# Kernel optimization log

Measured on AMD Instinct MI355X. Metric: run time of the kernel, lower is better.

## Reference

```python
import jax, jax.numpy as jnp
import numpy as np

H = 64
VOCAB = 64
THRESH_SCALE = 0.4
LN_EPS = 1e-5
NORM_EPS = 1e-12


def setup_inputs() -> dict:
    key = jax.random.key(0)
    ks = jax.random.split(key, 16)
    B, L = 64, 1024
    s = 1.0 / np.sqrt(H)
    inp = {
        "seq": jax.random.randint(ks[0], (B, L), 0, VOCAB),
        "embed_W": jax.random.normal(ks[1], (VOCAB, H), jnp.float32),
        "ff_W1": jax.random.normal(ks[2], (H, 2 * H), jnp.float32) * s,
        "ff_b1": jnp.zeros((2 * H,), jnp.float32),
        "ff_W2": jax.random.normal(ks[3], (2 * H, H), jnp.float32) * s,
        "ff_b2": jnp.zeros((H,), jnp.float32),
        "ln_g": jnp.ones((H,), jnp.float32),
        "ln_b": jnp.zeros((H,), jnp.float32),
        "kp_W": jax.random.normal(ks[4], (H, H), jnp.float32) * s,
        "vp_W": jax.random.normal(ks[5], (H, H), jnp.float32) * s,
        "qp_W": jax.random.normal(ks[6], (H, H), jnp.float32) * s,
        "rp_W": jax.random.normal(ks[7], (H, H), jnp.float32) * s,
        "rp_b": jnp.zeros((H,), jnp.float32),
        "out_W": jax.random.normal(ks[8], (H, VOCAB), jnp.float32) * s,
        "out_b": jnp.zeros((VOCAB,), jnp.float32),
    }
    return inp


def _forward(seq, embed_W, ff_W1, ff_b1, ff_W2, ff_b2, ln_g, ln_b,
             kp_W, vp_W, qp_W, rp_W, rp_b, out_W, out_b):
    h = embed_W[seq]                                    # [B, L, H]
    ff = jnp.maximum(h @ ff_W1 + ff_b1, 0.0) @ ff_W2 + ff_b2
    x = h + ff
    mu = x.mean(-1, keepdims=True)
    var = ((x - mu) ** 2).mean(-1, keepdims=True)       # biased var (torch LayerNorm)
    hn = (x - mu) / jnp.sqrt(var + LN_EPS) * ln_g + ln_b
    B, L, _ = hn.shape

    # Precompute all per-step keys/values, then scan the fast-weight update.
    k_all = hn[:, :-1] @ kp_W                           # [B, L-1, H]
    v_all = hn[:, :-1] @ vp_W                           # [B, L-1, H]
    kn_all = k_all / jnp.maximum(
        jnp.linalg.norm(k_all, axis=-1, keepdims=True), NORM_EPS)

    def step(M, kv):
        kn, v = kv                                      # each [B, H]
        vp = jnp.einsum('bij,bj->bi', M, kn)            # read M along k
        err = jnp.linalg.norm(v - vp, axis=-1)          # [B]
        gate = jnp.where(err > THRESH_SCALE * jnp.linalg.norm(v, axis=-1),
                         1.0, 0.0)                      # hard energy gate
        M = M + gate[:, None, None] * jnp.einsum('bi,bj->bij', v - vp, kn)
        return M, None

    M0 = jnp.zeros((B, H, H), dtype=hn.dtype)
    M, _ = jax.lax.scan(step, M0,
                        (kn_all.transpose(1, 0, 2), v_all.transpose(1, 0, 2)))

    q = hn[:, -1] @ qp_W                                # [B, H]
    r = jnp.einsum('bij,bj->bi', M, q) @ rp_W + rp_b
    return r @ out_W + out_b                            # [B, VOCAB]


def reference(seq, embed_W, ff_W1, ff_b1, ff_W2, ff_b2, ln_g, ln_b,
              kp_W, vp_W, qp_W, rp_W, rp_b, out_W, out_b):
    return _forward(seq, embed_W, ff_W1, ff_b1, ff_W2, ff_b2, ln_g, ln_b,
                    kp_W, vp_W, qp_W, rp_W, rp_b, out_W, out_b)
```

## Files before the change

### kernel.cpp

```cpp
#include <hip/hip_runtime.h>
#include <hip/hip_bf16.h>
#include <math.h>

#define BB 64
#define LL 1024
#define HH 64

typedef float v4f __attribute__((ext_vector_type(4)));
#define F4 __builtin_elementwise_fma

__global__ __launch_bounds__(256, 1)
void token_kernel(const int* __restrict__ seq,
                  const float* __restrict__ embed_W,
                  const float* __restrict__ ff_W1, const float* __restrict__ ff_b1,
                  const float* __restrict__ ff_W2, const float* __restrict__ ff_b2,
                  const float* __restrict__ ln_g, const float* __restrict__ ln_b,
                  const float* __restrict__ kp_W, const float* __restrict__ vp_W,
                  const float* __restrict__ qp_W,
                  float* __restrict__ knv, float* __restrict__ vthr,
                  float* __restrict__ qbuf)
{
    __shared__ __align__(16) float h_s[32][64];
    __shared__ __align__(16) float t1_s[32][128];
    __shared__ __align__(16) float hn_s[32][64];

    const int tid  = threadIdx.x;
    const int tok0 = blockIdx.x * 32;

#pragma unroll
    for (int k = 0; k < 8; ++k) {
        int e   = k * 256 + tid;
        int tok = e >> 6, i = e & 63;
        int s   = seq[tok0 + tok];
        h_s[tok][i] = embed_W[s * 64 + i];
    }
    __syncthreads();

    {
        const int j = tid & 127;
        const int g = tid >> 7;
        float w1c[64];
#pragma unroll
        for (int ii = 0; ii < 64; ++ii) w1c[ii] = ff_W1[ii * 128 + j];
        const float b1j = ff_b1[j];
#pragma unroll
        for (int tk = 0; tk < 16; ++tk) {
            const int tok = g * 16 + tk;
            const float4* h4 = (const float4*)h_s[tok];
            float a0 = b1j, a1 = 0.f, a2 = 0.f, a3 = 0.f;
#pragma unroll
            for (int w = 0; w < 16; ++w) {
                float4 hv = h4[w];
                a0 = fmaf(hv.x, w1c[4*w+0], a0);
                a1 = fmaf(hv.y, w1c[4*w+1], a1);
                a2 = fmaf(hv.z, w1c[4*w+2], a2);
                a3 = fmaf(hv.w, w1c[4*w+3], a3);
            }
            t1_s[tok][j] = fmaxf((a0 + a1) + (a2 + a3), 0.f);
        }
    }
    __syncthreads();

    {
        const int i  = tid & 63;
        const int w4 = tid >> 6;
        const float b2i = ff_b2[i];
        const float gi  = ln_g[i];
        const float bi  = ln_b[i];
        float accf[8];
#pragma unroll
        for (int tk = 0; tk < 8; ++tk) accf[tk] = b2i;
#pragma unroll
        for (int h = 0; h < 2; ++h) {
            float w2c[64];
#pragma unroll
            for (int jj = 0; jj < 64; ++jj) w2c[jj] = ff_W2[(h*64 + jj) * 64 + i];
#pragma unroll
            for (int tk = 0; tk < 8; ++tk) {
                const int tok = w4 * 8 + tk;
                const float4* t4 = (const float4*)&t1_s[tok][h*64];
                float a0 = 0.f, a1 = 0.f, a2 = 0.f, a3 = 0.f;
#pragma unroll
                for (int w = 0; w < 16; ++w) {
                    float4 tv = t4[w];
                    a0 = fmaf(tv.x, w2c[4*w+0], a0);
                    a1 = fmaf(tv.y, w2c[4*w+1], a1);
                    a2 = fmaf(tv.z, w2c[4*w+2], a2);
                    a3 = fmaf(tv.w, w2c[4*w+3], a3);
                }
                accf[tk] += (a0 + a1) + (a2 + a3);
            }
        }
#pragma unroll
        for (int tk = 0; tk < 8; ++tk) {
            const int tok = w4 * 8 + tk;
            float x = h_s[tok][i] + accf[tk];
            float s = x;
#pragma unroll
            for (int m = 32; m > 0; m >>= 1) s += __shfl_xor(s, m);
            float mu = s * (1.f / 64.f);
            float d  = x - mu;
            float s2 = d * d;
#pragma unroll
            for (int m = 32; m > 0; m >>= 1) s2 += __shfl_xor(s2, m);
            float var = s2 * (1.f / 64.f);
            hn_s[tok][i] = d / sqrtf(var + 1e-5f) * gi + bi;
        }
    }
    __syncthreads();

    {
        const int i  = tid & 63;
        const int w4 = tid >> 6;
        float kc[64], vc[64];
#pragma unroll
        for (int ii = 0; ii < 64; ++ii) {
            kc[ii] = kp_W[ii * 64 + i];
            vc[ii] = vp_W[ii * 64 + i];
        }
#pragma unroll
        for (int tk = 0; tk < 8; ++tk) {
            const int tok = w4 * 8 + tk;
            const int tg  = tok0 + tok;
            const int b   = tg >> 10;
            const int t   = tg & 1023;
            const float4* hn4 = (const float4*)hn_s[tok];
            if (t < 1023) {
                float ka0=0.f,ka1=0.f,ka2=0.f,ka3=0.f;
                float va0=0.f,va1=0.f,va2=0.f,va3=0.f;
#pragma unroll
                for (int w = 0; w < 16; ++w) {
                    float4 hv = hn4[w];
                    ka0 = fmaf(hv.x, kc[4*w+0], ka0);
                    ka1 = fmaf(hv.y, kc[4*w+1], ka1);
                    ka2 = fmaf(hv.z, kc[4*w+2], ka2);
                    ka3 = fmaf(hv.w, kc[4*w+3], ka3);
                    va0 = fmaf(hv.x, vc[4*w+0], va0);
                    va1 = fmaf(hv.y, vc[4*w+1], va1);
                    va2 = fmaf(hv.z, vc[4*w+2], va2);
                    va3 = fmaf(hv.w, vc[4*w+3], va3);
                }
                float ka = (ka0 + ka1) + (ka2 + ka3);
                float va = (va0 + va1) + (va2 + va3);
                float kn2 = ka * ka, vn2 = va * va;
#pragma unroll
                for (int m = 32; m > 0; m >>= 1) {
                    kn2 += __shfl_xor(kn2, m);
                    vn2 += __shfl_xor(vn2, m);
                }
                float knorm = fmaxf(sqrtf(kn2), 1e-12f);
                size_t row = ((size_t)b * 1024 + t) * 128;
                knv[row + i]      = ka / knorm;
                knv[row + 64 + i] = va;
                if (i == 0) vthr[b * 1024 + t] = 0.16f * vn2;
            } else {
                float qa0=0.f,qa1=0.f,qa2=0.f,qa3=0.f;
#pragma unroll
                for (int w = 0; w < 16; ++w) {
                    float4 hv = hn4[w];
                    qa0 = fmaf(hv.x, qp_W[(4*w+0)*64 + i], qa0);
                    qa1 = fmaf(hv.y, qp_W[(4*w+1)*64 + i], qa1);
                    qa2 = fmaf(hv.z, qp_W[(4*w+2)*64 + i], qa2);
                    qa3 = fmaf(hv.w, qp_W[(4*w+3)*64 + i], qa3);
                }
                qbuf[b * 64 + i] = (qa0 + qa1) + (qa2 + qa3);
            }
        }
    }
}


template<int CTRL>
__device__ __forceinline__ float dppadd(float x) {
    int y = __builtin_amdgcn_update_dpp(0, __float_as_int(x), CTRL, 0xF, 0xF, true);
    return x + __int_as_float(y);
}

__device__ __forceinline__ float wave_sum64(float x) {
    x = dppadd<0x111>(x); x = dppadd<0x112>(x);
    x = dppadd<0x114>(x); x = dppadd<0x118>(x);
    x = dppadd<0x142>(x); x = dppadd<0x143>(x);
    return __int_as_float(__builtin_amdgcn_readlane(__float_as_int(x), 63));
}

#define LOADK8(P, ROW) do { \
    const float* rA_ = (ROW) + (wid << 3); \
    const float* rB_ = rA_ + 4; \
    P##A0 = *(const v4f*)(rA_ +  0); P##A1 = *(const v4f*)(rA_ + 16); \
    P##A2 = *(const v4f*)(rA_ + 32); P##A3 = *(const v4f*)(rA_ + 48); \
    P##B0 = *(const v4f*)(rB_ +  0); P##B1 = *(const v4f*)(rB_ + 16); \
    P##B2 = *(const v4f*)(rB_ + 32); P##B3 = *(const v4f*)(rB_ + 48); \
} while (0)

#define UPD8(P) do { \
    v4f gv_ = {gd_s, gd_s, gd_s, gd_s}; \
    mA0 = F4(gv_, P##A0, mA0); mA1 = F4(gv_, P##A1, mA1); \
    mA2 = F4(gv_, P##A2, mA2); mA3 = F4(gv_, P##A3, mA3); \
    mB0 = F4(gv_, P##B0, mB0); mB1 = F4(gv_, P##B1, mB1); \
    mB2 = F4(gv_, P##B2, mB2); mB3 = F4(gv_, P##B3, mB3); \
} while (0)

#define ITER(X, Y, ROW2, TH2P2, P) do { \
    v4f po_ = ((const v4f*)pex[P][1 - wid])[lane];       \
    v4f sA_ = F4(mA0, X##A0, F4(mA1, X##A1, F4(mA2, X##A2, mA3 * X##A3))); \
    v4f sB_ = F4(mB0, X##B0, F4(mB1, X##B1, F4(mB2, X##B2, mB3 * X##B3))); \
    v4f pn_ = sA_ + sB_;                                 \
    float knl2_ = (ROW2)[lane]; \
    float vv2_  = (ROW2)[64 + lane]; \
    float t22_  = *(TH2P2); \
    v4f st_ = pown_prev + po_;                           \
    float base_ = (st_.x + st_.y) + (st_.z + st_.w); \
    float vp_ = fmaf(c_s, gd_s, base_); \
    float d_  = vv_s - vp_; \
    float e_  = wave_sum64(d_ * d_); \
    gd_s = (e_ > t2_s) ? d_ : 0.0f;                      \
    float cn_ = wave_sum64(knl_cur * knl_nxt); \
    UPD8(Y);                                             \
    LOADK8(Y, ROW2);                                     \
    ((v4f*)pex[(P) ^ 1][wid])[lane] = pn_;               \
    pown_prev = pn_; \
    c_s = cn_; knl_cur = knl_nxt; knl_nxt = knl2_; \
    vv_s = vv_nxt; vv_nxt = vv2_; t2_s = t2_nxt; t2_nxt = t22_; \
    asm volatile("s_waitcnt lgkmcnt(0)\n\ts_barrier" ::: "memory"); \
} while (0)

#define CHUNK16_W(CB, NB, TP) \
    ITER(S,T,(CB)+2*128,(TP)+2,0);   ITER(T,S,(CB)+3*128,(TP)+3,1); \
    ITER(S,T,(CB)+4*128,(TP)+4,0);   ITER(T,S,(CB)+5*128,(TP)+5,1); \
    ITER(S,T,(CB)+6*128,(TP)+6,0);   ITER(T,S,(CB)+7*128,(TP)+7,1); \
    ITER(S,T,(CB)+8*128,(TP)+8,0);   ITER(T,S,(CB)+9*128,(TP)+9,1); \
    ITER(S,T,(CB)+10*128,(TP)+10,0); ITER(T,S,(CB)+11*128,(TP)+11,1); \
    ITER(S,T,(CB)+12*128,(TP)+12,0); ITER(T,S,(CB)+13*128,(TP)+13,1); \
    ITER(S,T,(CB)+14*128,(TP)+14,0); ITER(T,S,(CB)+15*128,(TP)+15,1); \
    ITER(S,T,(NB)+0*128,(TP)+16,0);  ITER(T,S,(NB)+1*128,(TP)+17,1);

#define CHUNK15_W(CB, NB, TP) \
    ITER(S,T,(CB)+2*128,(TP)+2,0);   ITER(T,S,(CB)+3*128,(TP)+3,1); \
    ITER(S,T,(CB)+4*128,(TP)+4,0);   ITER(T,S,(CB)+5*128,(TP)+5,1); \
    ITER(S,T,(CB)+6*128,(TP)+6,0);   ITER(T,S,(CB)+7*128,(TP)+7,1); \
    ITER(S,T,(CB)+8*128,(TP)+8,0);   ITER(T,S,(CB)+9*128,(TP)+9,1); \
    ITER(S,T,(CB)+10*128,(TP)+10,0); ITER(T,S,(CB)+11*128,(TP)+11,1); \
    ITER(S,T,(CB)+12*128,(TP)+12,0); ITER(T,S,(CB)+13*128,(TP)+13,1); \
    ITER(S,T,(CB)+14*128,(TP)+14,0); ITER(T,S,(CB)+15*128,(TP)+15,1); \
    ITER(S,T,(NB)+0*128,(TP)+16,0);

__device__ __forceinline__ void gl2lds_1k(const float* g, float* l, int lane) {
    __builtin_amdgcn_global_load_lds(
        (const __attribute__((address_space(1))) void*)(g + lane * 4),
        (__attribute__((address_space(3))) void*)l, 16, 0, 0);
}

__device__ __forceinline__ void prefetch_half(const float* g, float* l,
                                              int lane, int wid) {
#pragma unroll
    for (int j = 0; j < 4; ++j)
        gl2lds_1k(g + wid * 1024 + j * 256, l + wid * 1024 + j * 256, lane);
}

__global__ __launch_bounds__(128, 1)
void scan_kernel(const float* __restrict__ knv,
                 const float* __restrict__ vthr,
                 const float* __restrict__ qbuf,
                 const float* __restrict__ rp_W, const float* __restrict__ rp_b,
                 const float* __restrict__ out_W, const float* __restrict__ out_b,
                 float* __restrict__ out)
{
    const int b    = blockIdx.x;
    const int tid  = threadIdx.x;
    const int lane = tid & 63;
    const int wid  = tid >> 6;
    const float* knvb = knv  + (size_t)b * 1024 * 128;
    const float* thrb = vthr + (size_t)b * 1024;

    __shared__ __align__(16) float thr_s[1040];
    __shared__ __align__(16) float buf[3 * 2048];
    __shared__ __align__(16) float pex[2][2][256];
    __shared__ float sh[64];

    v4f mA0={0,0,0,0},mA1={0,0,0,0},mA2={0,0,0,0},mA3={0,0,0,0};
    v4f mB0={0,0,0,0},mB1={0,0,0,0},mB2={0,0,0,0},mB3={0,0,0,0};
    v4f SA0,SA1,SA2,SA3,SB0,SB1,SB2,SB3;
    v4f TA0,TA1,TA2,TA3,TB0,TB1,TB2,TB3;

    if (wid == 0) {
#pragma unroll
        for (int w = 0; w < 4; ++w) gl2lds_1k(thrb + w * 256, thr_s + w * 256, lane);
    }
    prefetch_half(knvb,        buf,        lane, wid);
    prefetch_half(knvb + 2048, buf + 2048, lane, wid);
    prefetch_half(knvb + 4096, buf + 4096, lane, wid);

    {
        v4f z_ = {0.f, 0.f, 0.f, 0.f};
        ((v4f*)pex)[tid] = z_;
    }

    asm volatile("s_waitcnt vmcnt(4) lgkmcnt(0)\n\ts_barrier" ::: "memory");

    LOADK8(T, buf);
    LOADK8(S, buf + 128);
    v4f pown_prev = {0.f, 0.f, 0.f, 0.f};
    float knl_cur = buf[lane];
    float knl_nxt = buf[128 + lane];
    float vv_s    = buf[64 + lane];
    float vv_nxt  = buf[192 + lane];
    float t2_s    = thr_s[0];
    float t2_nxt  = thr_s[1];
    float gd_s = 0.f, c_s = 0.f;

#pragma unroll 1
    for (int c = 0; c < 62; ++c) {
        asm volatile("s_waitcnt vmcnt(4)" ::: "memory");
        const float* cb = buf + (c % 3) * 2048;
        const float* nb = buf + ((c + 1) % 3) * 2048;
        const float* tp = thr_s + c * 16;
        CHUNK16_W(cb, nb, tp)
        if (c <= 60)
            prefetch_half(knvb + (size_t)(c + 3) * 2048,
                          buf + (c % 3) * 2048, lane, wid);
    }
    asm volatile("s_waitcnt vmcnt(0)" ::: "memory");
    asm volatile("s_barrier" ::: "memory");
    {
        const float* cb = buf + 2 * 2048;
        const float* nb = buf;
        const float* tp = thr_s + 62 * 16;
        CHUNK16_W(cb, nb, tp)
    }
    {
        const float* cb = buf;
        const float* nb = buf + 2048;
        const float* tp = thr_s + 63 * 16;
        CHUNK15_W(cb, nb, tp)
    }

    {
        const v4f* qq = (const v4f*)(qbuf + b * 64);
        const int w2 = 2 * wid;
        v4f aqA = F4(mA0, qq[w2+0], F4(mA1, qq[w2+4],
                  F4(mA2, qq[w2+8],  mA3 * qq[w2+12])));
        v4f aqB = F4(mB0, qq[w2+1], F4(mB1, qq[w2+5],
                  F4(mB2, qq[w2+9],  mB3 * qq[w2+13])));
        v4f aq = aqA + aqB;
        float vq_own = (aq.x + aq.y) + (aq.z + aq.w);
        ((float*)pex)[wid * 64 + lane] = vq_own;
        asm volatile("s_waitcnt lgkmcnt(0)\n\ts_barrier" ::: "memory");
        float vq = vq_own + ((float*)pex)[(1 - wid) * 64 + lane];

        if (wid == 0) {
            sh[lane] = vq;
            asm volatile("s_waitcnt lgkmcnt(0)" ::: "memory");
            float r = rp_b[lane];
#pragma unroll
            for (int ii = 0; ii < 64; ++ii) r = fmaf(sh[ii], rp_W[ii * 64 + lane], r);
            asm volatile("s_waitcnt lgkmcnt(0)" ::: "memory");
            sh[lane] = r;
            asm volatile("s_waitcnt lgkmcnt(0)" ::: "memory");
            float o = out_b[lane];
#pragma unroll
            for (int ii = 0; ii < 64; ++ii) o = fmaf(sh[ii], out_W[ii * 64 + lane], o);
            out[b * 64 + lane] = o;
        }
    }
}

extern "C" void kernel_launch(void* const* d_in, const int* in_sizes, int n_in,
                              void* d_out, int out_size, void* d_ws, size_t ws_size,
                              hipStream_t stream)
{
    const int*   seq   = (const int*)  d_in[0];
    const float* embed = (const float*)d_in[1];
    const float* ffW1  = (const float*)d_in[2];
    const float* ffb1  = (const float*)d_in[3];
    const float* ffW2  = (const float*)d_in[4];
    const float* ffb2  = (const float*)d_in[5];
    const float* lng   = (const float*)d_in[6];
    const float* lnb   = (const float*)d_in[7];
    const float* kpW   = (const float*)d_in[8];
    const float* vpW   = (const float*)d_in[9];
    const float* qpW   = (const float*)d_in[10];
    const float* rpW   = (const float*)d_in[11];
    const float* rpb   = (const float*)d_in[12];
    const float* outW  = (const float*)d_in[13];
    const float* outb  = (const float*)d_in[14];
    float* out = (float*)d_out;

    float* knv  = (float*)d_ws;
    float* vthr = knv  + (size_t)64 * 1024 * 128;
    float* qbuf = vthr + (size_t)64 * 1024;

    token_kernel<<<2048, 256, 0, stream>>>(seq, embed, ffW1, ffb1, ffW2, ffb2,
                                           lng, lnb, kpW, vpW, qpW,
                                           knv, vthr, qbuf);
    scan_kernel<<<64, 128, 0, stream>>>(knv, vthr, qbuf,
                                        rpW, rpb, outW, outb, out);
}
```

Before: 417.0 us.

## Process two scan steps per barrier using algebraic correction for the second step

Restructures the fast-weight scan to handle two timesteps per iteration. Both matrix-vector reads are computed from the same M, and the second step's error and gate are corrected analytically through the key dot product c3, so the four wave reductions are batched into one interleaved DPP sweep. This halves the cross-wave LDS exchanges and barriers per step pair, at the cost of more registers for the extra double-buffered key sets and a slightly different floating-point evaluation order. The tail is changed to run a full eight-pair chunk, followed by a final pending update.

Result: faster. 368.6 us (-11.6%).

```diff
diff --git a/kernel.cpp b/kernel.cpp
--- a/kernel.cpp
+++ b/kernel.cpp
@@ -176,11 +176,25 @@
     return x + __int_as_float(y);
 }
 
+__device__ __forceinline__ float bcast63(float x) {
+    return __int_as_float(__builtin_amdgcn_readlane(__float_as_int(x), 63));
+}
+
 __device__ __forceinline__ float wave_sum64(float x) {
     x = dppadd<0x111>(x); x = dppadd<0x112>(x);
     x = dppadd<0x114>(x); x = dppadd<0x118>(x);
     x = dppadd<0x142>(x); x = dppadd<0x143>(x);
-    return __int_as_float(__builtin_amdgcn_readlane(__float_as_int(x), 63));
+    return bcast63(x);
+}
+
+__device__ __forceinline__ void wsum4(float& a, float& b, float& c, float& d) {
+    a = dppadd<0x111>(a); b = dppadd<0x111>(b); c = dppadd<0x111>(c); d = dppadd<0x111>(d);
+    a = dppadd<0x112>(a); b = dppadd<0x112>(b); c = dppadd<0x112>(c); d = dppadd<0x112>(d);
+    a = dppadd<0x114>(a); b = dppadd<0x114>(b); c = dppadd<0x114>(c); d = dppadd<0x114>(d);
+    a = dppadd<0x118>(a); b = dppadd<0x118>(b); c = dppadd<0x118>(c); d = dppadd<0x118>(d);
+    a = dppadd<0x142>(a); b = dppadd<0x142>(b); c = dppadd<0x142>(c); d = dppadd<0x142>(d);
+    a = dppadd<0x143>(a); b = dppadd<0x143>(b); c = dppadd<0x143>(c); d = dppadd<0x143>(d);
+    a = bcast63(a); b = bcast63(b); c = bcast63(c); d = bcast63(d);
 }
 
 #define LOADK8(P, ROW) do { \
@@ -192,57 +206,63 @@
     P##B2 = *(const v4f*)(rB_ + 32); P##B3 = *(const v4f*)(rB_ + 48); \
 } while (0)
 
-#define UPD8(P) do { \
-    v4f gv_ = {gd_s, gd_s, gd_s, gd_s}; \
+#define UPD8(P, G) do { \
+    v4f gv_ = {G, G, G, G}; \
     mA0 = F4(gv_, P##A0, mA0); mA1 = F4(gv_, P##A1, mA1); \
     mA2 = F4(gv_, P##A2, mA2); mA3 = F4(gv_, P##A3, mA3); \
     mB0 = F4(gv_, P##B0, mB0); mB1 = F4(gv_, P##B1, mB1); \
     mB2 = F4(gv_, P##B2, mB2); mB3 = F4(gv_, P##B3, mB3); \
 } while (0)
 
-#define ITER(X, Y, ROW2, TH2P2, P) do { \
-    v4f po_ = ((const v4f*)pex[P][1 - wid])[lane];       \
-    v4f sA_ = F4(mA0, X##A0, F4(mA1, X##A1, F4(mA2, X##A2, mA3 * X##A3))); \
-    v4f sB_ = F4(mB0, X##B0, F4(mB1, X##B1, F4(mB2, X##B2, mB3 * X##B3))); \
-    v4f pn_ = sA_ + sB_;                                 \
+#define CHUNK2(UP, UQ, XR, XS, ROW2, ROW3, TH2P, TH3P, PAR) do { \
+    UPD8(UP, gdp); \
+    UPD8(UQ, gdq); \
+    v4f qa_ = F4(mA0, XR##A0, F4(mA1, XR##A1, F4(mA2, XR##A2, mA3 * XR##A3))); \
+    v4f qb_ = F4(mB0, XR##B0, F4(mB1, XR##B1, F4(mB2, XR##B2, mB3 * XR##B3))); \
+    v4f q0_ = qa_ + qb_; \
+    float own0_ = (q0_.x + q0_.y) + (q0_.z + q0_.w); \
+    v4f ra_ = F4(mA0, XS##A0, F4(mA1, XS##A1, F4(mA2, XS##A2, mA3 * XS##A3))); \
+    v4f rb_ = F4(mB0, XS##B0, F4(mB1, XS##B1, F4(mB2, XS##B2, mB3 * XS##B3))); \
+    v4f r0_ = ra_ + rb_; \
+    float own1_ = (r0_.x + r0_.y) + (r0_.z + r0_.w); \
+    ((float2*)pex[PAR][wid])[lane] = make_float2(own0_, own1_); \
+    asm volatile("s_waitcnt lgkmcnt(0)\n\ts_barrier" ::: "memory"); \
+    float2 oth_ = ((const float2*)pex[PAR][1 - wid])[lane]; \
     float knl2_ = (ROW2)[lane]; \
+    float knl3_ = (ROW3)[lane]; \
     float vv2_  = (ROW2)[64 + lane]; \
-    float t22_  = *(TH2P2); \
-    v4f st_ = pown_prev + po_;                           \
-    float base_ = (st_.x + st_.y) + (st_.z + st_.w); \
-    float vp_ = fmaf(c_s, gd_s, base_); \
-    float d_  = vv_s - vp_; \
-    float e_  = wave_sum64(d_ * d_); \
-    gd_s = (e_ > t2_s) ? d_ : 0.0f;                      \
-    float cn_ = wave_sum64(knl_cur * knl_nxt); \
-    UPD8(Y);                                             \
-    LOADK8(Y, ROW2);                                     \
-    ((v4f*)pex[(P) ^ 1][wid])[lane] = pn_;               \
-    pown_prev = pn_; \
-    c_s = cn_; knl_cur = knl_nxt; knl_nxt = knl2_; \
-    vv_s = vv_nxt; vv_nxt = vv2_; t2_s = t2_nxt; t2_nxt = t22_; \
-    asm volatile("s_waitcnt lgkmcnt(0)\n\ts_barrier" ::: "memory"); \
+    float vv3_  = (ROW3)[64 + lane]; \
+    float th2_  = *(TH2P); \
+    float th3_  = *(TH3P); \
+    LOADK8(UP, ROW2); \
+    LOADK8(UQ, ROW3); \
+    float base0_ = own0_ + oth_.x; \
+    float base1_ = own1_ + oth_.y; \
+    float d00_ = vv0 - base0_; \
+    float d01_ = vv1 - base1_; \
+    float x0_ = d00_ * d00_, x1_ = d00_ * d01_; \
+    float x2_ = d01_ * d01_, x3_ = knl2_ * knl3_; \
+    wsum4(x0_, x1_, x2_, x3_); \
+    bool g0_ = x0_ > th0; \
+    float corr_ = fmaf(2.f * c3, x1_, -(c3 * c3) * x0_); \
+    float e1_ = g0_ ? (x2_ - corr_) : x2_; \
+    bool g1_ = e1_ > th1; \
+    float gd0_ = g0_ ? d00_ : 0.f; \
+    float d1_  = fmaf(-c3, gd0_, d01_); \
+    gdp = gd0_; \
+    gdq = g1_ ? d1_ : 0.f; \
+    vv0 = vv2_; vv1 = vv3_; th0 = th2_; th1 = th3_; c3 = x3_; \
 } while (0)
 
-#define CHUNK16_W(CB, NB, TP) \
-    ITER(S,T,(CB)+2*128,(TP)+2,0);   ITER(T,S,(CB)+3*128,(TP)+3,1); \
-    ITER(S,T,(CB)+4*128,(TP)+4,0);   ITER(T,S,(CB)+5*128,(TP)+5,1); \
-    ITER(S,T,(CB)+6*128,(TP)+6,0);   ITER(T,S,(CB)+7*128,(TP)+7,1); \
-    ITER(S,T,(CB)+8*128,(TP)+8,0);   ITER(T,S,(CB)+9*128,(TP)+9,1); \
-    ITER(S,T,(CB)+10*128,(TP)+10,0); ITER(T,S,(CB)+11*128,(TP)+11,1); \
-    ITER(S,T,(CB)+12*128,(TP)+12,0); ITER(T,S,(CB)+13*128,(TP)+13,1); \
-    ITER(S,T,(CB)+14*128,(TP)+14,0); ITER(T,S,(CB)+15*128,(TP)+15,1); \
-    ITER(S,T,(NB)+0*128,(TP)+16,0);  ITER(T,S,(NB)+1*128,(TP)+17,1);
-
-#define CHUNK15_W(CB, NB, TP) \
-    ITER(S,T,(CB)+2*128,(TP)+2,0);   ITER(T,S,(CB)+3*128,(TP)+3,1); \
-    ITER(S,T,(CB)+4*128,(TP)+4,0);   ITER(T,S,(CB)+5*128,(TP)+5,1); \
-    ITER(S,T,(CB)+6*128,(TP)+6,0);   ITER(T,S,(CB)+7*128,(TP)+7,1); \
-    ITER(S,T,(CB)+8*128,(TP)+8,0);   ITER(T,S,(CB)+9*128,(TP)+9,1); \
-    ITER(S,T,(CB)+10*128,(TP)+10,0); ITER(T,S,(CB)+11*128,(TP)+11,1); \
-    ITER(S,T,(CB)+12*128,(TP)+12,0); ITER(T,S,(CB)+13*128,(TP)+13,1); \
-    ITER(S,T,(CB)+14*128,(TP)+14,0); ITER(T,S,(CB)+15*128,(TP)+15,1); \
-    ITER(S,T,(NB)+0*128,(TP)+16,0);
+#define BUF8(CB, NB, TP) \
+    CHUNK2(U,V,S,T,(CB)+2*128, (CB)+3*128, (TP)+2, (TP)+3, 0); \
+    CHUNK2(S,T,U,V,(CB)+4*128, (CB)+5*128, (TP)+4, (TP)+5, 1); \
+    CHUNK2(U,V,S,T,(CB)+6*128, (CB)+7*128, (TP)+6, (TP)+7, 0); \
+    CHUNK2(S,T,U,V,(CB)+8*128, (CB)+9*128, (TP)+8, (TP)+9, 1); \
+    CHUNK2(U,V,S,T,(CB)+10*128,(CB)+11*128,(TP)+10,(TP)+11,0); \
+    CHUNK2(S,T,U,V,(CB)+12*128,(CB)+13*128,(TP)+12,(TP)+13,1); \
+    CHUNK2(U,V,S,T,(CB)+14*128,(CB)+15*128,(TP)+14,(TP)+15,0); \
+    CHUNK2(S,T,U,V,(NB)+0*128, (NB)+1*128, (TP)+16,(TP)+17,1);
 
 __device__ __forceinline__ void gl2lds_1k(const float* g, float* l, int lane) {
     __builtin_amdgcn_global_load_lds(
@@ -274,13 +294,15 @@
 
     __shared__ __align__(16) float thr_s[1040];
     __shared__ __align__(16) float buf[3 * 2048];
-    __shared__ __align__(16) float pex[2][2][256];
+    __shared__ __align__(16) float pex[2][2][128];
     __shared__ float sh[64];
 
     v4f mA0={0,0,0,0},mA1={0,0,0,0},mA2={0,0,0,0},mA3={0,0,0,0};
     v4f mB0={0,0,0,0},mB1={0,0,0,0},mB2={0,0,0,0},mB3={0,0,0,0};
     v4f SA0,SA1,SA2,SA3,SB0,SB1,SB2,SB3;
     v4f TA0,TA1,TA2,TA3,TB0,TB1,TB2,TB3;
+    v4f UA0,UA1,UA2,UA3,UB0,UB1,UB2,UB3;
+    v4f VA0,VA1,VA2,VA3,VB0,VB1,VB2,VB3;
 
     if (wid == 0) {
 #pragma unroll
@@ -290,23 +312,21 @@
     prefetch_half(knvb + 2048, buf + 2048, lane, wid);
     prefetch_half(knvb + 4096, buf + 4096, lane, wid);
 
+    asm volatile("s_waitcnt vmcnt(4) lgkmcnt(0)\n\ts_barrier" ::: "memory");
+
+    LOADK8(S, buf);
+    LOADK8(T, buf + 128);
     {
         v4f z_ = {0.f, 0.f, 0.f, 0.f};
-        ((v4f*)pex)[tid] = z_;
-    }
-
-    asm volatile("s_waitcnt vmcnt(4) lgkmcnt(0)\n\ts_barrier" ::: "memory");
-
-    LOADK8(T, buf);
-    LOADK8(S, buf + 128);
-    v4f pown_prev = {0.f, 0.f, 0.f, 0.f};
-    float knl_cur = buf[lane];
-    float knl_nxt = buf[128 + lane];
-    float vv_s    = buf[64 + lane];
-    float vv_nxt  = buf[192 + lane];
-    float t2_s    = thr_s[0];
-    float t2_nxt  = thr_s[1];
-    float gd_s = 0.f, c_s = 0.f;
+        UA0=z_;UA1=z_;UA2=z_;UA3=z_;UB0=z_;UB1=z_;UB2=z_;UB3=z_;
+        VA0=z_;VA1=z_;VA2=z_;VA3=z_;VB0=z_;VB1=z_;VB2=z_;VB3=z_;
+    }
+    float vv0 = buf[64 + lane];
+    float vv1 = buf[192 + lane];
+    float th0 = thr_s[0];
+    float th1 = thr_s[1];
+    float c3  = wave_sum64(buf[lane] * buf[128 + lane]);
+    float gdp = 0.f, gdq = 0.f;
 
 #pragma unroll 1
     for (int c = 0; c < 62; ++c) {
@@ -314,7 +334,7 @@
         const float* cb = buf + (c % 3) * 2048;
         const float* nb = buf + ((c + 1) % 3) * 2048;
         const float* tp = thr_s + c * 16;
-        CHUNK16_W(cb, nb, tp)
+        BUF8(cb, nb, tp)
         if (c <= 60)
             prefetch_half(knvb + (size_t)(c + 3) * 2048,
                           buf + (c % 3) * 2048, lane, wid);
@@ -325,14 +345,15 @@
         const float* cb = buf + 2 * 2048;
         const float* nb = buf;
         const float* tp = thr_s + 62 * 16;
-        CHUNK16_W(cb, nb, tp)
+        BUF8(cb, nb, tp)
     }
     {
         const float* cb = buf;
         const float* nb = buf + 2048;
         const float* tp = thr_s + 63 * 16;
-        CHUNK15_W(cb, nb, tp)
-    }
+        BUF8(cb, nb, tp)
+    }
+    UPD8(U, gdp);
 
     {
         const v4f* qq = (const v4f*)(qbuf + b * 64);
```
